# Kernel optimization log

Hardware: AMD Instinct MI355X
Metric: run time of the kernel (lower is better)

The kernel has to match this reference:

```python
import jax, jax.numpy as jnp
import numpy as np

DIM = 512        # embed dim (num_heads=4 -> head_dim=128)
PROJ = 128       # proj_dim
NLAYERS = 3      # conv layers
EXT = 64         # attnExtension
NPOS = 8         # ceil(log2(2*EXT+5))
HEADS = 4
S = 2048         # source sequence length; target length = 5*S
KDIM = PROJ + NPOS


def setup_inputs() -> dict:
    key = jax.random.key(0)
    ks = jax.random.split(key, 10)
    def w(k, shape, s=0.02):
        return jax.random.normal(k, shape, jnp.float32) * s
    return {
        "x": jax.random.normal(ks[0], (S, PROJ), jnp.float32),
        "residual": jax.random.normal(ks[1], (5 * S, DIM), jnp.float32),
        "proj_w": w(ks[2], (DIM * 5, KDIM)),
        "proj_b": jnp.zeros((DIM * 5,), jnp.float32),
        "q_w": w(ks[3], (DIM, DIM)),
        "k_w": w(ks[4], (DIM, KDIM)),
        "v_w": w(ks[5], (DIM, KDIM)),
        "in_b": jnp.zeros((3 * DIM,), jnp.float32),
        "out_w": w(ks[6], (DIM, DIM)),
        "out_b": jnp.zeros((DIM,), jnp.float32),
        "conv_w": w(ks[7], (NLAYERS, DIM, DIM, 3)),
        "conv_b": jnp.zeros((NLAYERS, DIM), jnp.float32),
        "skip_w": w(ks[8], (DIM, DIM)),
        "skip_b": jnp.zeros((DIM,), jnp.float32),
    }


def _layernorm(z):
    # elementwise_affine=False, eps=1e-5, normalize over last dim
    m = jnp.mean(z, axis=-1, keepdims=True)
    v = jnp.mean((z - m) ** 2, axis=-1, keepdims=True)
    return (z - m) * jax.lax.rsqrt(v + 1e-5)


def _forward(x, residual, proj_w, proj_b, q_w, k_w, v_w, in_b, out_w, out_b,
             conv_w, conv_b, skip_w, skip_b):
    s = x.shape[0]
    hd = DIM // HEADS
    # positional embeddings: pos[:, i] = (arange(S) % 2**(i+1)) / 2**i
    n = jnp.arange(s)[:, None]
    exps = jnp.arange(NPOS)
    pos = (n % (2 ** (exps + 1))).astype(jnp.float32) / (2.0 ** exps).astype(jnp.float32)
    src = jnp.concatenate([x, pos], axis=1)                     # [S, KDIM]
    tgt = (src @ proj_w.T + proj_b).reshape(-1, DIM)            # [5S, DIM]
    L = 5 * s
    # multihead attention (eval mode: dropout off)
    q = (tgt @ q_w.T + in_b[:DIM]).reshape(L, HEADS, hd)
    k = (src @ k_w.T + in_b[DIM:2 * DIM]).reshape(s, HEADS, hd)
    v = (src @ v_w.T + in_b[2 * DIM:]).reshape(s, HEADS, hd)
    scores = jnp.einsum('lhd,shd->hls', q, k) / jnp.sqrt(jnp.float32(hd))
    # banded mask: query l may attend source i iff 5i-EXT <= l < 5(i+1)+EXT
    rows = jnp.arange(L)[:, None]
    cols = jnp.arange(s)[None, :]
    allowed = (rows >= 5 * cols - EXT) & (rows < 5 * cols + 5 + EXT)   # [5S, S]
    scores = jnp.where(allowed[None], scores, jnp.float32(-1e30))
    attn = jax.nn.softmax(scores, axis=-1)
    o = jnp.einsum('hls,shd->lhd', attn, v).reshape(L, DIM)
    attn_out = o @ out_w.T + out_b
    cnn_input = _layernorm(attn_out) + residual                 # [5S, DIM]
    # conv1d stack (unbatched, channels=DIM, length=5S), softplus each layer
    h = cnn_input.T[None]                                       # [1, DIM, 5S]
    for li in range(NLAYERS):
        h = jax.lax.conv_general_dilated(
            h, conv_w[li], window_strides=(1,), padding=[(1, 1)],
            dimension_numbers=('NCH', 'OIH', 'NCH'))
        h = jax.nn.softplus(h + conv_b[li][None, :, None])
    out = _layernorm(h[0].T + (cnn_input @ skip_w.T + skip_b))
    return out


def reference(x, residual, proj_w, proj_b, q_w, k_w, v_w, in_b, out_w, out_b,
              conv_w, conv_b, skip_w, skip_b):
    return _forward(x, residual, proj_w, proj_b, q_w, k_w, v_w, in_b, out_w,
                    out_b, conv_w, conv_b, skip_w, skip_b)
```

## Files before the change

kernel.cpp:

```cpp
#include <hip/hip_runtime.h>
#include <hip/hip_bf16.h>


#define S_LEN   2048
#define S_PAD   32
#define L_LEN   10240
#define DIM     512
#define KDIM    136
#define KDIM_P  192
#define NPOS    8
#define HEADS   4
#define HDIM    128
#define NLAYERS 3
#define CONV_K  1536
#define KV_LD   1024
#define CS_LD   68

typedef __attribute__((ext_vector_type(8))) short bf16x8;
typedef __attribute__((ext_vector_type(4))) float f32x4;

__device__ __forceinline__ float softplus_f(float x) {
    if (x > 15.0f) return x;
    return __logf(1.0f + __expf(x));
}

__device__ __forceinline__ void gload_lds16(const __hip_bfloat16* g,
                                            __hip_bfloat16* l) {
    __builtin_amdgcn_global_load_lds(
        (const __attribute__((address_space(1))) void*)g,
        (__attribute__((address_space(3))) void*)l, 16, 0, 0);
}

template<bool SOFTPLUS, bool OUT_BF16>
__global__ __launch_bounds__(256) void gemm_bk64(
    const __hip_bfloat16* __restrict__ A, int lda,
    const __hip_bfloat16* __restrict__ W, int ldw,
    const float* __restrict__ bias,
    __hip_bfloat16* __restrict__ Cb, float* __restrict__ Cf, int ldc,
    int K)
{
    __shared__ __align__(16) char smem[49152];
    __hip_bfloat16* As = (__hip_bfloat16*)smem;
    __hip_bfloat16* Bs = (__hip_bfloat16*)(smem + 32768);
    float*          Cs = (float*)smem;

    const int t = threadIdx.x;
    const int w = t >> 6;
    const int lane = t & 63;
    const int r16 = lane & 15;
    const int quad = lane >> 4;

    const int m0 = blockIdx.x * 128;
    const int n0 = blockIdx.y * 64;
    const int mo = (w >> 1) * 64;
    const int no = (w & 1) * 32;

    const int srow = w * 16 + (lane >> 2);
    const int scol = (lane & 3) * 8;
    const __hip_bfloat16* Ag0 = A + (size_t)(m0 + srow) * lda + scol;
    const __hip_bfloat16* Ag1 = A + (size_t)(m0 + 64 + srow) * lda + scol;
    const __hip_bfloat16* Wg  = W + (size_t)(n0 + srow) * ldw + scol;
    __hip_bfloat16* lA0 = &As[(size_t)(w * 16) * 32];
    __hip_bfloat16* lA1 = &As[(size_t)(64 + w * 16) * 32];
    __hip_bfloat16* lB  = &Bs[(size_t)(w * 16) * 32];

    f32x4 acc[4][2];
    #pragma unroll
    for (int i = 0; i < 4; ++i)
        #pragma unroll
        for (int j = 0; j < 2; ++j)
            acc[i][j] = (f32x4){0.f, 0.f, 0.f, 0.f};

    const int NK = K >> 6;

    auto stage = [&](int buf, int k0) {
        #pragma unroll
        for (int kh = 0; kh < 2; ++kh) {
            const int gk = k0 + kh * 32;
            gload_lds16(Ag0 + gk, lA0 + buf * 8192 + kh * 4096);
            gload_lds16(Ag1 + gk, lA1 + buf * 8192 + kh * 4096);
            gload_lds16(Wg  + gk, lB  + buf * 4096 + kh * 2048);
        }
    };

    stage(0, 0);

    for (int k = 0; k < NK; ++k) {
        const int buf = k & 1;
        if (k + 1 < NK) {
            stage(buf ^ 1, (k + 1) << 6);
            asm volatile("s_waitcnt vmcnt(6)" ::: "memory");
        } else {
            asm volatile("s_waitcnt vmcnt(0)" ::: "memory");
        }
        asm volatile("s_barrier" ::: "memory");

        #pragma unroll
        for (int kh = 0; kh < 2; ++kh) {
            const __hip_bfloat16* Asb = As + buf * 8192 + kh * 4096;
            const __hip_bfloat16* Bsb = Bs + buf * 4096 + kh * 2048;
            bf16x8 af[4], bfr[2];
            #pragma unroll
            for (int i = 0; i < 4; ++i)
                af[i] = *(const bf16x8*)&Asb[(mo + i * 16 + r16) * 32 + quad * 8];
            #pragma unroll
            for (int j = 0; j < 2; ++j)
                bfr[j] = *(const bf16x8*)&Bsb[(no + j * 16 + r16) * 32 + quad * 8];
            #pragma unroll
            for (int i = 0; i < 4; ++i)
                #pragma unroll
                for (int j = 0; j < 2; ++j)
                    acc[i][j] = __builtin_amdgcn_mfma_f32_16x16x32_bf16(
                        af[i], bfr[j], acc[i][j], 0, 0, 0);
        }

        asm volatile("s_waitcnt lgkmcnt(0)" ::: "memory");
        asm volatile("s_barrier" ::: "memory");
    }

    #pragma unroll
    for (int i = 0; i < 4; ++i) {
        const int rl = mo + i * 16 + quad * 4;
        #pragma unroll
        for (int j = 0; j < 2; ++j) {
            const int cl = no + j * 16 + r16;
            const float bs = bias[n0 + cl];
            #pragma unroll
            for (int r = 0; r < 4; ++r) {
                float v = acc[i][j][r] + bs;
                if (SOFTPLUS) v = softplus_f(v);
                Cs[(rl + r) * CS_LD + cl] = v;
            }
        }
    }
    __syncthreads();

    if (OUT_BF16) {
        const int rsub = lane >> 3;
        const int c8 = (lane & 7) * 8;
        #pragma unroll
        for (int it = 0; it < 4; ++it) {
            const int rl = w * 32 + it * 8 + rsub;
            const float* src = &Cs[rl * CS_LD + c8];
            f32x4 a = *(const f32x4*)src;
            f32x4 b = *(const f32x4*)(src + 4);
            bf16x8 o;
            #pragma unroll
            for (int e = 0; e < 4; ++e) {
                __hip_bfloat16 x = __float2bfloat16(a[e]);
                __hip_bfloat16 y = __float2bfloat16(b[e]);
                o[e]     = *(short*)&x;
                o[e + 4] = *(short*)&y;
            }
            *(bf16x8*)(Cb + (size_t)(m0 + rl) * ldc + n0 + c8) = o;
        }
    } else {
        const int rsub = lane >> 4;
        const int c4 = (lane & 15) * 4;
        #pragma unroll
        for (int it = 0; it < 8; ++it) {
            const int rl = w * 32 + it * 4 + rsub;
            f32x4 a = *(const f32x4*)&Cs[rl * CS_LD + c4];
            *(f32x4*)(Cf + (size_t)(m0 + rl) * ldc + n0 + c4) = a;
        }
    }
}

#define VT_STRIDE 40

__global__ __launch_bounds__(256) void attn_mfma_kernel(
    const __hip_bfloat16* __restrict__ qb,
    const __hip_bfloat16* __restrict__ kb,
    const __hip_bfloat16* __restrict__ vb,
    __hip_bfloat16* __restrict__ ob)
{
    __shared__ __hip_bfloat16 Vt[HEADS][HDIM * VT_STRIDE];
    __shared__ __hip_bfloat16 Ps[HEADS][16 * 32];

    const int t = threadIdx.x;
    const int h = t >> 6;
    const int lane = t & 63;
    const int r16 = lane & 15;
    const int quad = lane >> 4;
    const int l0 = blockIdx.x * 16;

    int i_start = (l0 - 64) / 5;
    if (i_start < 0) i_start = 0;

    {
        const int s = lane & 31;
        const int half = lane >> 5;
        const __hip_bfloat16* vrow =
            vb + (size_t)(i_start + s) * KV_LD + h * HDIM + half * 64;
        short* vt = (short*)Vt[h];
        #pragma unroll
        for (int jj = 0; jj < 8; ++jj) {
            bf16x8 v = *(const bf16x8*)(vrow + jj * 8);
            #pragma unroll
            for (int e = 0; e < 8; ++e)
                vt[(half * 64 + jj * 8 + e) * VT_STRIDE + s] = v[e];
        }
    }

    const short* qg = (const short*)qb + (size_t)(l0 + r16) * DIM + h * HDIM + quad * 8;
    const short* kg0 = (const short*)kb + (size_t)(i_start + r16) * KV_LD + h * HDIM + quad * 8;
    const short* kg1 = kg0 + 16 * KV_LD;

    f32x4 c0 = {0.f, 0.f, 0.f, 0.f};
    f32x4 c1 = {0.f, 0.f, 0.f, 0.f};
    #pragma unroll
    for (int kk = 0; kk < 4; ++kk) {
        bf16x8 aq = *(const bf16x8*)(qg + kk * 32);
        bf16x8 b0 = *(const bf16x8*)(kg0 + kk * 32);
        bf16x8 b1 = *(const bf16x8*)(kg1 + kk * 32);
        c0 = __builtin_amdgcn_mfma_f32_16x16x32_bf16(aq, b0, c0, 0, 0, 0);
        c1 = __builtin_amdgcn_mfma_f32_16x16x32_bf16(aq, b1, c1, 0, 0, 0);
    }

    const float scale = 0.08838834764831845f;
    const int ic0 = i_start + r16;
    const int ic1 = ic0 + 16;
    float recl[4];
    short* ps = (short*)Ps[h];
    #pragma unroll
    for (int r = 0; r < 4; ++r) {
        const int l = l0 + quad * 4 + r;
        const bool a0 = (l >= 5 * ic0 - 64) && (l < 5 * ic0 + 69) && (ic0 < S_LEN);
        const bool a1 = (l >= 5 * ic1 - 64) && (l < 5 * ic1 + 69) && (ic1 < S_LEN);
        float s0 = a0 ? c0[r] * scale : -1e30f;
        float s1 = a1 ? c1[r] * scale : -1e30f;
        float mx = fmaxf(s0, s1);
        #pragma unroll
        for (int o = 8; o; o >>= 1) mx = fmaxf(mx, __shfl_xor(mx, o));
        float e0 = __expf(s0 - mx);
        float e1 = __expf(s1 - mx);
        float sm = e0 + e1;
        #pragma unroll
        for (int o = 8; o; o >>= 1) sm += __shfl_xor(sm, o);
        recl[r] = 1.0f / sm;
        __hip_bfloat16 p0 = __float2bfloat16(e0);
        __hip_bfloat16 p1 = __float2bfloat16(e1);
        ps[(quad * 4 + r) * 32 + r16]      = *(short*)&p0;
        ps[(quad * 4 + r) * 32 + r16 + 16] = *(short*)&p1;
    }

    __syncthreads();

    bf16x8 ap = *(const bf16x8*)&Ps[h][r16 * 32 + quad * 8];
    #pragma unroll
    for (int nt = 0; nt < 8; ++nt) {
        bf16x8 bv = *(const bf16x8*)&Vt[h][(nt * 16 + r16) * VT_STRIDE + quad * 8];
        f32x4 o = {0.f, 0.f, 0.f, 0.f};
        o = __builtin_amdgcn_mfma_f32_16x16x32_bf16(ap, bv, o, 0, 0, 0);
        #pragma unroll
        for (int r = 0; r < 4; ++r) {
            ob[(size_t)(l0 + quad * 4 + r) * DIM + h * HDIM + nt * 16 + r16] =
                __float2bfloat16(o[r] * recl[r]);
        }
    }
}

__global__ __launch_bounds__(256) void ln_residual_kernel(
    const float* __restrict__ attn_out, const float* __restrict__ residual,
    __hip_bfloat16* __restrict__ hp0)
{
    __shared__ float red[4];
    const int r = blockIdx.x;
    const int t = threadIdx.x;
    const size_t base = (size_t)r * DIM + t * 2;
    float z0 = attn_out[base], z1 = attn_out[base + 1];

    float s = z0 + z1;
    #pragma unroll
    for (int o = 32; o; o >>= 1) s += __shfl_xor(s, o);
    if ((t & 63) == 0) red[t >> 6] = s;
    __syncthreads();
    const float mean = (red[0] + red[1] + red[2] + red[3]) * (1.0f / DIM);
    __syncthreads();

    const float d0 = z0 - mean, d1 = z1 - mean;
    float vq = d0 * d0 + d1 * d1;
    #pragma unroll
    for (int o = 32; o; o >>= 1) vq += __shfl_xor(vq, o);
    if ((t & 63) == 0) red[t >> 6] = vq;
    __syncthreads();
    const float var = (red[0] + red[1] + red[2] + red[3]) * (1.0f / DIM);
    const float rstd = rsqrtf(var + 1e-5f);

    const float y0 = d0 * rstd + residual[base];
    const float y1 = d1 * rstd + residual[base + 1];
    __hip_bfloat16* out = hp0 + (size_t)(r + 1) * DIM + t * 2;
    out[0] = __float2bfloat16(y0);
    out[1] = __float2bfloat16(y1);
}

__global__ __launch_bounds__(256) void final_ln_kernel(
    const float* __restrict__ conv_out, const float* __restrict__ skip_out,
    float* __restrict__ out)
{
    __shared__ float red[4];
    const int r = blockIdx.x;
    const int t = threadIdx.x;
    const size_t base = (size_t)r * DIM + t * 2;
    float z0 = conv_out[base] + skip_out[base];
    float z1 = conv_out[base + 1] + skip_out[base + 1];

    float s = z0 + z1;
    #pragma unroll
    for (int o = 32; o; o >>= 1) s += __shfl_xor(s, o);
    if ((t & 63) == 0) red[t >> 6] = s;
    __syncthreads();
    const float mean = (red[0] + red[1] + red[2] + red[3]) * (1.0f / DIM);
    __syncthreads();

    const float d0 = z0 - mean, d1 = z1 - mean;
    float vq = d0 * d0 + d1 * d1;
    #pragma unroll
    for (int o = 32; o; o >>= 1) vq += __shfl_xor(vq, o);
    if ((t & 63) == 0) red[t >> 6] = vq;
    __syncthreads();
    const float var = (red[0] + red[1] + red[2] + red[3]) * (1.0f / DIM);
    const float rstd = rsqrtf(var + 1e-5f);

    out[base]     = d0 * rstd;
    out[base + 1] = d1 * rstd;
}

__global__ void build_src_kernel(const float* __restrict__ x,
                                 __hip_bfloat16* __restrict__ src)
{
    int idx = blockIdx.x * 256 + threadIdx.x;
    if (idx >= S_LEN * KDIM_P) return;
    int i = idx / KDIM_P, j = idx % KDIM_P;
    float v;
    if (j < 128)       v = x[i * 128 + j];
    else if (j < KDIM) { int e = j - 128; v = (float)(i & ((2 << e) - 1)) / (float)(1 << e); }
    else               v = 0.f;
    src[idx] = __float2bfloat16(v);
}

__global__ void convert_pad_kernel(const float* __restrict__ src,
                                   __hip_bfloat16* __restrict__ dst,
                                   int R, int C, int Cp)
{
    int idx = blockIdx.x * 256 + threadIdx.x;
    if (idx >= R * Cp) return;
    int r = idx / Cp, c = idx % Cp;
    dst[idx] = __float2bfloat16(c < C ? src[(size_t)r * C + c] : 0.f);
}

__global__ void conv_wt_kernel(const float* __restrict__ w,
                               __hip_bfloat16* __restrict__ wt)
{
    int idx = blockIdx.x * 256 + threadIdx.x;
    if (idx >= NLAYERS * DIM * CONV_K) return;
    int lc = idx / CONV_K;
    int rem = idx % CONV_K;
    int k = rem / DIM, ci = rem % DIM;
    wt[idx] = __float2bfloat16(w[(size_t)lc * CONV_K + ci * 3 + k]);
}

__global__ void zero_pad_rows_kernel(__hip_bfloat16* hp0, __hip_bfloat16* hp1)
{
    const int t = threadIdx.x;
    const __hip_bfloat16 z = __float2bfloat16(0.f);
    if      (blockIdx.x == 0) hp0[t] = z;
    else if (blockIdx.x == 1) hp0[(size_t)(L_LEN + 1) * DIM + t] = z;
    else if (blockIdx.x == 2) hp1[t] = z;
    else                      hp1[(size_t)(L_LEN + 1) * DIM + t] = z;
}

__global__ void zero_kv_pad_kernel(__hip_bfloat16* kv_b)
{
    int idx = blockIdx.x * 256 + threadIdx.x;
    if (idx >= S_PAD * KV_LD) return;
    kv_b[(size_t)S_LEN * KV_LD + idx] = __float2bfloat16(0.f);
}

extern "C" void kernel_launch(void* const* d_in, const int* in_sizes, int n_in,
                              void* d_out, int out_size, void* d_ws, size_t ws_size,
                              hipStream_t stream)
{
    const float* x        = (const float*)d_in[0];
    const float* residual = (const float*)d_in[1];
    const float* proj_w   = (const float*)d_in[2];
    const float* proj_b   = (const float*)d_in[3];
    const float* q_w      = (const float*)d_in[4];
    const float* k_w      = (const float*)d_in[5];
    const float* v_w      = (const float*)d_in[6];
    const float* in_b     = (const float*)d_in[7];
    const float* out_w    = (const float*)d_in[8];
    const float* out_b    = (const float*)d_in[9];
    const float* conv_w   = (const float*)d_in[10];
    const float* conv_b   = (const float*)d_in[11];
    const float* skip_w   = (const float*)d_in[12];
    const float* skip_b   = (const float*)d_in[13];
    float* out = (float*)d_out;

    char* ws = (char*)d_ws;
    size_t off = 0;
    auto alloc = [&](size_t bytes) { char* p = ws + off; off += (bytes + 255) & ~(size_t)255; return p; };

    __hip_bfloat16* src_b   = (__hip_bfloat16*)alloc((size_t)S_LEN * KDIM_P * 2);
    __hip_bfloat16* projw_b = (__hip_bfloat16*)alloc((size_t)DIM * 5 * KDIM_P * 2);
    __hip_bfloat16* qw_b    = (__hip_bfloat16*)alloc((size_t)DIM * DIM * 2);
    __hip_bfloat16* kvw_b   = (__hip_bfloat16*)alloc((size_t)KV_LD * KDIM_P * 2);
    __hip_bfloat16* outw_b  = (__hip_bfloat16*)alloc((size_t)DIM * DIM * 2);
    __hip_bfloat16* skipw_b = (__hip_bfloat16*)alloc((size_t)DIM * DIM * 2);
    __hip_bfloat16* convwt  = (__hip_bfloat16*)alloc((size_t)NLAYERS * DIM * CONV_K * 2);
    __hip_bfloat16* tgt_b   = (__hip_bfloat16*)alloc((size_t)L_LEN * DIM * 2);
    __hip_bfloat16* q_b     = (__hip_bfloat16*)alloc((size_t)L_LEN * DIM * 2);
    __hip_bfloat16* kv_b    = (__hip_bfloat16*)alloc((size_t)(S_LEN + S_PAD) * KV_LD * 2);
    __hip_bfloat16* o_b     = (__hip_bfloat16*)alloc((size_t)L_LEN * DIM * 2);
    float*          attn_f  = (float*)alloc((size_t)L_LEN * DIM * 4);
    __hip_bfloat16* hp0     = (__hip_bfloat16*)alloc((size_t)(L_LEN + 2) * DIM * 2);
    __hip_bfloat16* hp1     = (__hip_bfloat16*)alloc((size_t)(L_LEN + 2) * DIM * 2);
    float*          conv_f  = (float*)alloc((size_t)L_LEN * DIM * 4);
    float*          skip_f  = attn_f;
    (void)ws_size; (void)n_in; (void)in_sizes; (void)out_size;

    build_src_kernel<<<(S_LEN * KDIM_P + 255) / 256, 256, 0, stream>>>(x, src_b);
    convert_pad_kernel<<<(DIM * 5 * KDIM_P + 255) / 256, 256, 0, stream>>>(proj_w, projw_b, DIM * 5, KDIM, KDIM_P);
    convert_pad_kernel<<<(DIM * DIM + 255) / 256, 256, 0, stream>>>(q_w, qw_b, DIM, DIM, DIM);
    convert_pad_kernel<<<(DIM * KDIM_P + 255) / 256, 256, 0, stream>>>(k_w, kvw_b, DIM, KDIM, KDIM_P);
    convert_pad_kernel<<<(DIM * KDIM_P + 255) / 256, 256, 0, stream>>>(v_w, kvw_b + (size_t)DIM * KDIM_P, DIM, KDIM, KDIM_P);
    convert_pad_kernel<<<(DIM * DIM + 255) / 256, 256, 0, stream>>>(out_w, outw_b, DIM, DIM, DIM);
    convert_pad_kernel<<<(DIM * DIM + 255) / 256, 256, 0, stream>>>(skip_w, skipw_b, DIM, DIM, DIM);
    conv_wt_kernel<<<(NLAYERS * DIM * CONV_K + 255) / 256, 256, 0, stream>>>(conv_w, convwt);
    zero_pad_rows_kernel<<<4, 512, 0, stream>>>(hp0, hp1);
    zero_kv_pad_kernel<<<(S_PAD * KV_LD + 255) / 256, 256, 0, stream>>>(kv_b);

    gemm_bk64<false, true><<<dim3(S_LEN / 128, DIM * 5 / 64), 256, 0, stream>>>(
        src_b, KDIM_P, projw_b, KDIM_P, proj_b, tgt_b, nullptr, DIM * 5, KDIM_P);
    gemm_bk64<false, true><<<dim3(L_LEN / 128, DIM / 64), 256, 0, stream>>>(
        tgt_b, DIM, qw_b, DIM, in_b, q_b, nullptr, DIM, DIM);
    gemm_bk64<false, true><<<dim3(S_LEN / 128, KV_LD / 64), 256, 0, stream>>>(
        src_b, KDIM_P, kvw_b, KDIM_P, in_b + DIM, kv_b, nullptr, KV_LD, KDIM_P);

    attn_mfma_kernel<<<L_LEN / 16, 256, 0, stream>>>(q_b, kv_b, kv_b + DIM, o_b);

    gemm_bk64<false, false><<<dim3(L_LEN / 128, DIM / 64), 256, 0, stream>>>(
        o_b, DIM, outw_b, DIM, out_b, nullptr, attn_f, DIM, DIM);

    ln_residual_kernel<<<L_LEN, 256, 0, stream>>>(attn_f, residual, hp0);

    gemm_bk64<false, false><<<dim3(L_LEN / 128, DIM / 64), 256, 0, stream>>>(
        hp0 + DIM, DIM, skipw_b, DIM, skip_b, nullptr, skip_f, DIM, DIM);

    gemm_bk64<true, true><<<dim3(L_LEN / 128, DIM / 64), 256, 0, stream>>>(
        hp0, DIM, convwt, CONV_K, conv_b, hp1 + DIM, nullptr, DIM, CONV_K);
    gemm_bk64<true, true><<<dim3(L_LEN / 128, DIM / 64), 256, 0, stream>>>(
        hp1, DIM, convwt + (size_t)DIM * CONV_K, CONV_K, conv_b + DIM, hp0 + DIM, nullptr, DIM, CONV_K);
    gemm_bk64<true, false><<<dim3(L_LEN / 128, DIM / 64), 256, 0, stream>>>(
        hp0, DIM, convwt + (size_t)2 * DIM * CONV_K, CONV_K, conv_b + 2 * DIM, nullptr, conv_f, DIM, CONV_K);

    final_ln_kernel<<<L_LEN, 256, 0, stream>>>(conv_f, skip_f, out);
}
```

Measured before the change: 298.0 us.

## Fold q projection into input projection weights and merge QKV GEMMs

Precomputes combined weights Wq·Wproj_j for each of the five target chunks so q is computed directly from src (K=192) instead of materializing tgt and running a K=512 GEMM over 10240 rows. Q, K and V projections are merged into one GEMM with a split epilogue writing to q_b and kv_b, and the ten staging kernels are merged into one launch. This removes the tgt buffer round-trip and most of the q-projection FLOPs, at the cost of a small weight-product GEMM, a serial-loop bias kernel, and different bf16 rounding from the folded weights.

```diff
diff --git a/kernel.cpp b/kernel.cpp
--- a/kernel.cpp
+++ b/kernel.cpp
@@ -8,13 +8,13 @@
 #define DIM     512
 #define KDIM    136
 #define KDIM_P  192
-#define NPOS    8
 #define HEADS   4
 #define HDIM    128
 #define NLAYERS 3
 #define CONV_K  1536
 #define KV_LD   1024
 #define CS_LD   68
+#define NQKV    3584
 
 typedef __attribute__((ext_vector_type(8))) short bf16x8;
 typedef __attribute__((ext_vector_type(4))) float f32x4;
@@ -31,18 +31,23 @@
         (__attribute__((address_space(3))) void*)l, 16, 0, 0);
 }
 
-template<bool SOFTPLUS, bool OUT_BF16>
+template<bool SOFTPLUS, bool OUT_BF16, bool QKV>
 __global__ __launch_bounds__(256) void gemm_bk64(
     const __hip_bfloat16* __restrict__ A, int lda,
     const __hip_bfloat16* __restrict__ W, int ldw,
     const float* __restrict__ bias,
     __hip_bfloat16* __restrict__ Cb, float* __restrict__ Cf, int ldc,
-    int K)
+    int K, long az, long wz, long cz,
+    __hip_bfloat16* __restrict__ qdst, __hip_bfloat16* __restrict__ kvdst)
 {
     __shared__ __align__(16) char smem[49152];
     __hip_bfloat16* As = (__hip_bfloat16*)smem;
     __hip_bfloat16* Bs = (__hip_bfloat16*)(smem + 32768);
     float*          Cs = (float*)smem;
+
+    A  += (size_t)blockIdx.z * az;
+    W  += (size_t)blockIdx.z * wz;
+    if (OUT_BF16) Cb += (size_t)blockIdx.z * cz;
 
     const int t = threadIdx.x;
     const int w = t >> 6;
@@ -138,6 +143,14 @@
     if (OUT_BF16) {
         const int rsub = lane >> 3;
         const int c8 = (lane & 7) * 8;
+        __hip_bfloat16* base;
+        long rstride;
+        if (QKV) {
+            if (n0 < 2560) { base = qdst + n0;          rstride = 2560; }
+            else           { base = kvdst + (n0 - 2560); rstride = KV_LD; }
+        } else {
+            base = Cb + n0; rstride = ldc;
+        }
         #pragma unroll
         for (int it = 0; it < 4; ++it) {
             const int rl = w * 32 + it * 8 + rsub;
@@ -152,7 +165,7 @@
                 o[e]     = *(short*)&x;
                 o[e + 4] = *(short*)&y;
             }
-            *(bf16x8*)(Cb + (size_t)(m0 + rl) * ldc + n0 + c8) = o;
+            *(bf16x8*)(base + (size_t)(m0 + rl) * rstride + c8) = o;
         }
     } else {
         const int rsub = lane >> 4;
@@ -326,55 +339,104 @@
     out[base + 1] = d1 * rstd;
 }
 
-__global__ void build_src_kernel(const float* __restrict__ x,
-                                 __hip_bfloat16* __restrict__ src)
+#define SG0 (S_LEN * KDIM_P)
+#define SG1 (5 * KDIM_P * DIM)
+#define SG2 (DIM * DIM)
+#define SG3 (KV_LD * KDIM_P)
+#define SG4 (DIM * DIM)
+#define SG5 (DIM * DIM)
+#define SG6 (NLAYERS * DIM * CONV_K)
+#define SG7 (S_PAD * KV_LD)
+#define SG8 (4 * DIM)
+#define SG9 (4096)
+#define SG_TOTAL (SG0+SG1+SG2+SG3+SG4+SG5+SG6+SG7+SG8+SG9)
+
+__global__ void stage_all_kernel(
+    const float* __restrict__ x, const float* __restrict__ proj_w,
+    const float* __restrict__ q_w, const float* __restrict__ k_w,
+    const float* __restrict__ v_w, const float* __restrict__ out_w,
+    const float* __restrict__ skip_w, const float* __restrict__ conv_w,
+    __hip_bfloat16* src_b, __hip_bfloat16* projw_T, __hip_bfloat16* qw_b,
+    __hip_bfloat16* W_all, __hip_bfloat16* outw_b, __hip_bfloat16* skipw_b,
+    __hip_bfloat16* convwt, __hip_bfloat16* kv_b,
+    __hip_bfloat16* hp0, __hip_bfloat16* hp1, float* zeros)
 {
     int idx = blockIdx.x * 256 + threadIdx.x;
-    if (idx >= S_LEN * KDIM_P) return;
-    int i = idx / KDIM_P, j = idx % KDIM_P;
-    float v;
-    if (j < 128)       v = x[i * 128 + j];
-    else if (j < KDIM) { int e = j - 128; v = (float)(i & ((2 << e) - 1)) / (float)(1 << e); }
-    else               v = 0.f;
-    src[idx] = __float2bfloat16(v);
-}
-
-__global__ void convert_pad_kernel(const float* __restrict__ src,
-                                   __hip_bfloat16* __restrict__ dst,
-                                   int R, int C, int Cp)
-{
-    int idx = blockIdx.x * 256 + threadIdx.x;
-    if (idx >= R * Cp) return;
-    int r = idx / Cp, c = idx % Cp;
-    dst[idx] = __float2bfloat16(c < C ? src[(size_t)r * C + c] : 0.f);
-}
-
-__global__ void conv_wt_kernel(const float* __restrict__ w,
-                               __hip_bfloat16* __restrict__ wt)
-{
-    int idx = blockIdx.x * 256 + threadIdx.x;
-    if (idx >= NLAYERS * DIM * CONV_K) return;
-    int lc = idx / CONV_K;
-    int rem = idx % CONV_K;
-    int k = rem / DIM, ci = rem % DIM;
-    wt[idx] = __float2bfloat16(w[(size_t)lc * CONV_K + ci * 3 + k]);
-}
-
-__global__ void zero_pad_rows_kernel(__hip_bfloat16* hp0, __hip_bfloat16* hp1)
-{
-    const int t = threadIdx.x;
-    const __hip_bfloat16 z = __float2bfloat16(0.f);
-    if      (blockIdx.x == 0) hp0[t] = z;
-    else if (blockIdx.x == 1) hp0[(size_t)(L_LEN + 1) * DIM + t] = z;
-    else if (blockIdx.x == 2) hp1[t] = z;
-    else                      hp1[(size_t)(L_LEN + 1) * DIM + t] = z;
-}
-
-__global__ void zero_kv_pad_kernel(__hip_bfloat16* kv_b)
-{
-    int idx = blockIdx.x * 256 + threadIdx.x;
-    if (idx >= S_PAD * KV_LD) return;
-    kv_b[(size_t)S_LEN * KV_LD + idx] = __float2bfloat16(0.f);
+    if (idx >= SG_TOTAL) return;
+    const __hip_bfloat16 zb = __float2bfloat16(0.f);
+
+    if (idx < SG0) {
+        int i = idx / KDIM_P, j = idx % KDIM_P;
+        float v;
+        if (j < 128)       v = x[i * 128 + j];
+        else if (j < KDIM) { int e = j - 128; v = (float)(i & ((2 << e) - 1)) / (float)(1 << e); }
+        else               v = 0.f;
+        src_b[idx] = __float2bfloat16(v);
+        return;
+    }
+    idx -= SG0;
+    if (idx < SG1) {
+        int j = idx / (KDIM_P * DIM);
+        int rem = idx % (KDIM_P * DIM);
+        int k = rem / DIM, d = rem % DIM;
+        projw_T[idx] = (k < KDIM)
+            ? __float2bfloat16(proj_w[(size_t)(j * DIM + d) * KDIM + k]) : zb;
+        return;
+    }
+    idx -= SG1;
+    if (idx < SG2) { qw_b[idx] = __float2bfloat16(q_w[idx]); return; }
+    idx -= SG2;
+    if (idx < SG3) {
+        int r = idx / KDIM_P, c = idx % KDIM_P;
+        float v = 0.f;
+        if (c < KDIM) v = (r < DIM) ? k_w[(size_t)r * KDIM + c]
+                                    : v_w[(size_t)(r - DIM) * KDIM + c];
+        W_all[(size_t)(2560 + r) * KDIM_P + c] = __float2bfloat16(v);
+        return;
+    }
+    idx -= SG3;
+    if (idx < SG4) { outw_b[idx] = __float2bfloat16(out_w[idx]); return; }
+    idx -= SG4;
+    if (idx < SG5) { skipw_b[idx] = __float2bfloat16(skip_w[idx]); return; }
+    idx -= SG5;
+    if (idx < SG6) {
+        int lc = idx / CONV_K;
+        int rem = idx % CONV_K;
+        int k = rem / DIM, ci = rem % DIM;
+        convwt[idx] = __float2bfloat16(conv_w[(size_t)lc * CONV_K + ci * 3 + k]);
+        return;
+    }
+    idx -= SG6;
+    if (idx < SG7) { kv_b[(size_t)S_LEN * KV_LD + idx] = zb; return; }
+    idx -= SG7;
+    if (idx < SG8) {
+        int t = idx % DIM, which = idx / DIM;
+        if      (which == 0) hp0[t] = zb;
+        else if (which == 1) hp0[(size_t)(L_LEN + 1) * DIM + t] = zb;
+        else if (which == 2) hp1[t] = zb;
+        else                 hp1[(size_t)(L_LEN + 1) * DIM + t] = zb;
+        return;
+    }
+    idx -= SG8;
+    zeros[idx] = 0.f;
+}
+
+__global__ void bias_all_kernel(const float* __restrict__ q_w,
+                                const float* __restrict__ proj_b,
+                                const float* __restrict__ in_b,
+                                float* __restrict__ bias_all)
+{
+    int n = blockIdx.x * 256 + threadIdx.x;
+    if (n >= NQKV) return;
+    if (n < 2560) {
+        int j = n / DIM, c = n % DIM;
+        float s = in_b[c];
+        for (int d = 0; d < DIM; ++d)
+            s += q_w[(size_t)c * DIM + d] * proj_b[j * DIM + d];
+        bias_all[n] = s;
+    } else {
+        bias_all[n] = in_b[DIM + (n - 2560)];
+    }
 }
 
 extern "C" void kernel_launch(void* const* d_in, const int* in_sizes, int n_in,
@@ -402,13 +464,14 @@
     auto alloc = [&](size_t bytes) { char* p = ws + off; off += (bytes + 255) & ~(size_t)255; return p; };
 
     __hip_bfloat16* src_b   = (__hip_bfloat16*)alloc((size_t)S_LEN * KDIM_P * 2);
-    __hip_bfloat16* projw_b = (__hip_bfloat16*)alloc((size_t)DIM * 5 * KDIM_P * 2);
+    __hip_bfloat16* projw_T = (__hip_bfloat16*)alloc((size_t)5 * KDIM_P * DIM * 2);
     __hip_bfloat16* qw_b    = (__hip_bfloat16*)alloc((size_t)DIM * DIM * 2);
-    __hip_bfloat16* kvw_b   = (__hip_bfloat16*)alloc((size_t)KV_LD * KDIM_P * 2);
+    __hip_bfloat16* W_all   = (__hip_bfloat16*)alloc((size_t)NQKV * KDIM_P * 2);
     __hip_bfloat16* outw_b  = (__hip_bfloat16*)alloc((size_t)DIM * DIM * 2);
     __hip_bfloat16* skipw_b = (__hip_bfloat16*)alloc((size_t)DIM * DIM * 2);
     __hip_bfloat16* convwt  = (__hip_bfloat16*)alloc((size_t)NLAYERS * DIM * CONV_K * 2);
-    __hip_bfloat16* tgt_b   = (__hip_bfloat16*)alloc((size_t)L_LEN * DIM * 2);
+    float*          zeros   = (float*)alloc(4096 * 4);
+    float*          bias_qkv= (float*)alloc(NQKV * 4);
     __hip_bfloat16* q_b     = (__hip_bfloat16*)alloc((size_t)L_LEN * DIM * 2);
     __hip_bfloat16* kv_b    = (__hip_bfloat16*)alloc((size_t)(S_LEN + S_PAD) * KV_LD * 2);
     __hip_bfloat16* o_b     = (__hip_bfloat16*)alloc((size_t)L_LEN * DIM * 2);
@@ -419,40 +482,42 @@
     float*          skip_f  = attn_f;
     (void)ws_size; (void)n_in; (void)in_sizes; (void)out_size;
 
-    build_src_kernel<<<(S_LEN * KDIM_P + 255) / 256, 256, 0, stream>>>(x, src_b);
-    convert_pad_kernel<<<(DIM * 5 * KDIM_P + 255) / 256, 256, 0, stream>>>(proj_w, projw_b, DIM * 5, KDIM, KDIM_P);
-    convert_pad_kernel<<<(DIM * DIM + 255) / 256, 256, 0, stream>>>(q_w, qw_b, DIM, DIM, DIM);
-    convert_pad_kernel<<<(DIM * KDIM_P + 255) / 256, 256, 0, stream>>>(k_w, kvw_b, DIM, KDIM, KDIM_P);
-    convert_pad_kernel<<<(DIM * KDIM_P + 255) / 256, 256, 0, stream>>>(v_w, kvw_b + (size_t)DIM * KDIM_P, DIM, KDIM, KDIM_P);
-    convert_pad_kernel<<<(DIM * DIM + 255) / 256, 256, 0, stream>>>(out_w, outw_b, DIM, DIM, DIM);
-    convert_pad_kernel<<<(DIM * DIM + 255) / 256, 256, 0, stream>>>(skip_w, skipw_b, DIM, DIM, DIM);
-    conv_wt_kernel<<<(NLAYERS * DIM * CONV_K + 255) / 256, 256, 0, stream>>>(conv_w, convwt);
-    zero_pad_rows_kernel<<<4, 512, 0, stream>>>(hp0, hp1);
-    zero_kv_pad_kernel<<<(S_PAD * KV_LD + 255) / 256, 256, 0, stream>>>(kv_b);
-
-    gemm_bk64<false, true><<<dim3(S_LEN / 128, DIM * 5 / 64), 256, 0, stream>>>(
-        src_b, KDIM_P, projw_b, KDIM_P, proj_b, tgt_b, nullptr, DIM * 5, KDIM_P);
-    gemm_bk64<false, true><<<dim3(L_LEN / 128, DIM / 64), 256, 0, stream>>>(
-        tgt_b, DIM, qw_b, DIM, in_b, q_b, nullptr, DIM, DIM);
-    gemm_bk64<false, true><<<dim3(S_LEN / 128, KV_LD / 64), 256, 0, stream>>>(
-        src_b, KDIM_P, kvw_b, KDIM_P, in_b + DIM, kv_b, nullptr, KV_LD, KDIM_P);
+    stage_all_kernel<<<(SG_TOTAL + 255) / 256, 256, 0, stream>>>(
+        x, proj_w, q_w, k_w, v_w, out_w, skip_w, conv_w,
+        src_b, projw_T, qw_b, W_all, outw_b, skipw_b, convwt, kv_b,
+        hp0, hp1, zeros);
+    bias_all_kernel<<<(NQKV + 255) / 256, 256, 0, stream>>>(
+        q_w, proj_b, in_b, bias_qkv);
+
+    gemm_bk64<false, true, false><<<dim3(4, KDIM_P / 64, 5), 256, 0, stream>>>(
+        qw_b, DIM, projw_T, DIM, zeros, W_all, nullptr, KDIM_P, DIM,
+        0, (long)KDIM_P * DIM, (long)DIM * KDIM_P, nullptr, nullptr);
+
+    gemm_bk64<false, true, true><<<dim3(S_LEN / 128, NQKV / 64), 256, 0, stream>>>(
+        src_b, KDIM_P, W_all, KDIM_P, bias_qkv, nullptr, nullptr, 0, KDIM_P,
+        0, 0, 0, q_b, kv_b);
 
     attn_mfma_kernel<<<L_LEN / 16, 256, 0, stream>>>(q_b, kv_b, kv_b + DIM, o_b);
 
-    gemm_bk64<false, false><<<dim3(L_LEN / 128, DIM / 64), 256, 0, stream>>>(
-        o_b, DIM, outw_b, DIM, out_b, nullptr, attn_f, DIM, DIM);
+    gemm_bk64<false, false, false><<<dim3(L_LEN / 128, DIM / 64), 256, 0, stream>>>(
+        o_b, DIM, outw_b, DIM, out_b, nullptr, attn_f, DIM, DIM,
+        0, 0, 0, nullptr, nullptr);
 
     ln_residual_kernel<<<L_LEN, 256, 0, stream>>>(attn_f, residual, hp0);
 
-    gemm_bk64<false, false><<<dim3(L_LEN / 128, DIM / 64), 256, 0, stream>>>(
-        hp0 + DIM, DIM, skipw_b, DIM, skip_b, nullptr, skip_f, DIM, DIM);
-
-    gemm_bk64<true, true><<<dim3(L_LEN / 128, DIM / 64), 256, 0, stream>>>(
-        hp0, DIM, convwt, CONV_K, conv_b, hp1 + DIM, nullptr, DIM, CONV_K);
-    gemm_bk64<true, true><<<dim3(L_LEN / 128, DIM / 64), 256, 0, stream>>>(
-        hp1, DIM, convwt + (size_t)DIM * CONV_K, CONV_K, conv_b + DIM, hp0 + DIM, nullptr, DIM, CONV_K);
-    gemm_bk64<true, false><<<dim3(L_LEN / 128, DIM / 64), 256, 0, stream>>>(
-        hp0, DIM, convwt + (size_t)2 * DIM * CONV_K, CONV_K, conv_b + 2 * DIM, nullptr, conv_f, DIM, CONV_K);
+    gemm_bk64<false, false, false><<<dim3(L_LEN / 128, DIM / 64), 256, 0, stream>>>(
+        hp0 + DIM, DIM, skipw_b, DIM, skip_b, nullptr, skip_f, DIM, DIM,
+        0, 0, 0, nullptr, nullptr);
+
+    gemm_bk64<true, true, false><<<dim3(L_LEN / 128, DIM / 64), 256, 0, stream>>>(
+        hp0, DIM, convwt, CONV_K, conv_b, hp1 + DIM, nullptr, DIM, CONV_K,
+        0, 0, 0, nullptr, nullptr);
+    gemm_bk64<true, true, false><<<dim3(L_LEN / 128, DIM / 64), 256, 0, stream>>>(
+        hp1, DIM, convwt + (size_t)DIM * CONV_K, CONV_K, conv_b + DIM, hp0 + DIM, nullptr, DIM, CONV_K,
+        0, 0, 0, nullptr, nullptr);
+    gemm_bk64<true, false, false><<<dim3(L_LEN / 128, DIM / 64), 256, 0, stream>>>(
+        hp0, DIM, convwt + (size_t)2 * DIM * CONV_K, CONV_K, conv_b + 2 * DIM, nullptr, conv_f, DIM, CONV_K,
+        0, 0, 0, nullptr, nullptr);
 
     final_ln_kernel<<<L_LEN, 256, 0, stream>>>(conv_f, skip_f, out);
 }
```

Measured after the change: 295.8 us. Within noise of the previous version (-0.7%).
